# Kernel optimization log

Measured on AMD Instinct MI355X. Metric: run time of the kernel, lower is better.

Reference implementation:

```python
import jax, jax.numpy as jnp
import numpy as np

B, S, D = 4, 2048, 1024
H = 16
HD = D // H  # head dim = 64


def setup_inputs() -> dict:
    key = jax.random.key(0)
    ks = jax.random.split(key, 9)
    s = 1.0 / np.sqrt(D)
    return {
        "Q": jax.random.normal(ks[0], (B, S, D), dtype=jnp.float32),
        "K": jax.random.normal(ks[1], (B, S, D), dtype=jnp.float32),
        "V": jax.random.normal(ks[2], (B, S, D), dtype=jnp.float32),
        "Wq": jax.random.uniform(ks[3], (D, D), jnp.float32, -s, s),
        "bq": jax.random.uniform(ks[4], (D,), jnp.float32, -s, s),
        "Wk": jax.random.uniform(ks[5], (D, D), jnp.float32, -s, s),
        "bk": jax.random.uniform(ks[6], (D,), jnp.float32, -s, s),
        "Wv": jax.random.uniform(ks[7], (D, D), jnp.float32, -s, s),
        "bv": jax.random.uniform(ks[8], (D,), jnp.float32, -s, s),
    }


def reference(Q, K, V, Wq, bq, Wk, bk, Wv, bv):
    # Linear projections, split into heads: (B, H, S, HD)
    def proj(x, W, b):
        y = x @ W + b  # torch Linear uses x @ W.T; here W is stored pre-transposed (D_in, D_out)
        return y.reshape(B, S, H, HD).transpose(0, 2, 1, 3)

    q = proj(Q, Wq, bq)
    k = proj(K, Wk, bk)
    v = proj(V, Wv, bv)

    scale = 1.0 / jnp.sqrt(jnp.float32(HD))
    scores = jnp.einsum("bhqd,bhkd->bhqk", q, k) * scale  # (B,H,S,S)
    # causal mask (mask=True path): -inf above the diagonal
    causal = jnp.triu(jnp.full((S, S), -jnp.inf, dtype=scores.dtype), k=1)
    scores = scores + causal
    attn = jax.nn.softmax(scores, axis=-1)
    ctx = jnp.einsum("bhqk,bhkd->bhqd", attn, v)  # (B,H,S,HD)
    return ctx.transpose(0, 2, 1, 3).reshape(B, S, H * HD)
```

## Files before the change

### kernel.cpp

```cpp
#include <hip/hip_runtime.h>
#include <hip/hip_bf16.h>
#include <stdint.h>

#define B_  4
#define S_  2048
#define D_  1024
#define H_  16
#define HD_ 64
#define LOG2E 1.44269504088896f

typedef unsigned short u16;
typedef short bf16x8 __attribute__((ext_vector_type(8)));
typedef float f32x4 __attribute__((ext_vector_type(4)));

static __device__ __forceinline__ u16 f2bf(float f) {
    union { float f; uint32_t u; } v; v.f = f;
    return (u16)((v.u + 0x7FFF + ((v.u >> 16) & 1)) >> 16);
}

static __device__ __forceinline__ uint32_t cvt_pk_bf16(float lo, float hi) {
    uint32_t r;
    asm("v_cvt_pk_bf16_f32 %0, %1, %2" : "=v"(r) : "v"(lo), "v"(hi));
    return r;
}

static __device__ __forceinline__ uint32_t pk2(float lo, float hi) {
    return __builtin_amdgcn_perm(__float_as_uint(hi), __float_as_uint(lo), 0x07060302u);
}

static __device__ __forceinline__ bf16x8 rd_swz(const u16* base, int row, int slot) {
    return *(const bf16x8*)((const char*)base + row * 128 + ((slot ^ (row & 7)) << 4));
}

static __device__ __forceinline__ void gll_swz(const u16* grow0, size_t stride,
                                               u16* lds_chunk, int lane) {
    const int r = lane >> 3;
    const int slot = (lane & 7) ^ r;
    const u16* g = grow0 + (size_t)r * stride + slot * 8;
    __builtin_amdgcn_global_load_lds(
        (const __attribute__((address_space(1))) uint32_t*)g,
        (__attribute__((address_space(3))) uint32_t*)lds_chunk, 16, 0, 0);
}

__global__ __launch_bounds__(256) void wtrans(
    const float* __restrict__ W0, const float* __restrict__ W1, const float* __restrict__ W2,
    u16* __restrict__ T0, u16* __restrict__ T1, u16* __restrict__ T2)
{
    const float* W = blockIdx.z == 0 ? W0 : (blockIdx.z == 1 ? W1 : W2);
    u16* T       = blockIdx.z == 0 ? T0 : (blockIdx.z == 1 ? T1 : T2);
    __shared__ float t[32][33];
    const int n0 = blockIdx.x * 32, k0 = blockIdx.y * 32;
    const int tx = threadIdx.x, ty = threadIdx.y;
#pragma unroll
    for (int i = 0; i < 4; ++i)
        t[ty + i * 8][tx] = W[(size_t)(k0 + ty + i * 8) * D_ + n0 + tx];
    __syncthreads();
#pragma unroll
    for (int i = 0; i < 4; ++i)
        T[(size_t)(n0 + ty + i * 8) * D_ + k0 + tx] = f2bf(t[tx][ty + i * 8]);
}

template <int MODE>
__global__ __launch_bounds__(256) void proj_gemm(
    const float* __restrict__ X, const u16* __restrict__ Wt,
    const float* __restrict__ bias, u16* __restrict__ out)
{
    __shared__ __align__(16) u16 lA[128 * 64];
    __shared__ __align__(16) u16 lB[128 * 64];
    const int tid = threadIdx.x;
    const int m0 = blockIdx.x * 128, n0 = blockIdx.y * 128;
    const int w = tid >> 6, lane = tid & 63;
    const int lr = lane & 15, lg = lane >> 4;
    const int wr = (w >> 1) * 64, wc = (w & 1) * 64;

    f32x4 acc[4][4] = {};

    for (int k0 = 0; k0 < D_; k0 += 64) {
        __syncthreads();
#pragma unroll
        for (int i = 0; i < 4; ++i) {
            const int c = w * 4 + i;
            gll_swz(Wt + (size_t)(n0 + c * 8) * D_ + k0, D_, &lB[c * 512], lane);
        }
#pragma unroll
        for (int i = 0; i < 8; ++i) {
            const int lin = i * 1024 + tid * 4;
            const int r = lin >> 6, c = lin & 63;
            const float4 v = *(const float4*)(X + (size_t)(m0 + r) * D_ + k0 + c);
            uint2 pk;
            pk.x = pk2(v.x, v.y);
            pk.y = pk2(v.z, v.w);
            const int phys = r * 128 + (((c >> 3) ^ (r & 7)) << 4) + ((c & 7) << 1);
            *(uint2*)((char*)lA + phys) = pk;
        }
        __syncthreads();
#pragma unroll
        for (int kk = 0; kk < 64; kk += 32) {
            bf16x8 af[4], bfr[4];
#pragma unroll
            for (int m = 0; m < 4; ++m)
                af[m] = rd_swz(lA, wr + m * 16 + lr, (kk >> 3) + lg);
#pragma unroll
            for (int n = 0; n < 4; ++n)
                bfr[n] = rd_swz(lB, wc + n * 16 + lr, (kk >> 3) + lg);
#pragma unroll
            for (int m = 0; m < 4; ++m)
#pragma unroll
                for (int n = 0; n < 4; ++n)
                    acc[m][n] = __builtin_amdgcn_mfma_f32_16x16x32_bf16(af[m], bfr[n], acc[m][n], 0, 0, 0);
        }
    }
#pragma unroll
    for (int m = 0; m < 4; ++m)
#pragma unroll
        for (int n = 0; n < 4; ++n)
#pragma unroll
            for (int j = 0; j < 4; ++j) {
                const int gm = m0 + wr + m * 16 + lg * 4 + j;
                const int gn = n0 + wc + n * 16 + lr;
                float y = acc[m][n][j] + bias[gn];
                if (MODE == 0) y *= 0.125f * LOG2E;
                const int bb = gm >> 11, s = gm & (S_ - 1);
                const int h = gn >> 6, hd = gn & 63;
                size_t off;
                if (MODE < 2) off = (((size_t)bb * H_ + h) * S_ + s) * HD_ + hd;
                else {
                    const int s6 = s & 63;
                    const int sp = (s & ~63) | (s6 & 0x20) | ((s6 & 0xC) << 1) |
                                   ((s6 & 0x10) >> 2) | (s6 & 3);
                    off = (((size_t)bb * H_ + h) * HD_ + hd) * S_ + sp;
                }
                out[off] = f2bf(y);
            }
}

__global__ __launch_bounds__(512) void attn_kernel(
    const u16* __restrict__ qb, const u16* __restrict__ kb,
    const u16* __restrict__ vtb, float* __restrict__ out)
{
    const int bh = blockIdx.y;
    const int b = bh >> 4, h = bh & 15;
    const int tid = threadIdx.x;
    const int w = tid >> 6, lane = tid & 63;
    const int lr = lane & 15, lg = lane >> 4;

    __shared__ __align__(16) u16 lK[64 * 64];
    __shared__ __align__(16) u16 lV[64 * 64];

    const size_t kbase = (size_t)bh * S_ * HD_;
    const size_t vbase = (size_t)bh * HD_ * S_;

    for (int e = 0; e < 2; ++e) {
        const int qi = (e == 0) ? (int)blockIdx.x : 15 - (int)blockIdx.x;
        const int q0 = qi * 128;
        const int qrow = q0 + w * 16 + lr;

        const size_t qoff = ((size_t)bh * S_ + qrow) * HD_;
        const bf16x8 qf0 = *(const bf16x8*)(qb + qoff + lg * 8);
        const bf16x8 qf1 = *(const bf16x8*)(qb + qoff + 32 + lg * 8);

        f32x4 oacc[4] = {};
        float l_run = 0.f;

        const int tmax = 2 * qi + 1;
        for (int t = 0; t <= tmax; ++t) {
            const int kv0 = t * 64;
            __syncthreads();
            gll_swz(kb + kbase + (size_t)(kv0 + w * 8) * HD_, HD_, &lK[w * 512], lane);
            gll_swz(vtb + vbase + (size_t)(w * 8) * S_ + kv0, S_, &lV[w * 512], lane);
            __syncthreads();

            if (t == tmax && w < 4) continue;

            f32x4 sacc[4];
            __builtin_amdgcn_s_setprio(1);
#pragma unroll
            for (int n = 0; n < 4; ++n) {
                const bf16x8 k0f = rd_swz(lK, n * 16 + lr, lg);
                const bf16x8 k1f = rd_swz(lK, n * 16 + lr, 4 + lg);
                f32x4 z = {};
                z = __builtin_amdgcn_mfma_f32_16x16x32_bf16(k0f, qf0, z, 0, 0, 0);
                z = __builtin_amdgcn_mfma_f32_16x16x32_bf16(k1f, qf1, z, 0, 0, 0);
                sacc[n] = z;
            }
            __builtin_amdgcn_s_setprio(0);

            if (t >= tmax - 1) {
#pragma unroll
                for (int n = 0; n < 4; ++n)
#pragma unroll
                    for (int j = 0; j < 4; ++j)
                        if (kv0 + n * 16 + lg * 4 + j > qrow) sacc[n][j] = -1e30f;
            }

            float g[16];
#pragma unroll
            for (int n = 0; n < 4; ++n)
#pragma unroll
                for (int j = 0; j < 4; ++j) {
                    const float p = exp2f(sacc[n][j]);
                    sacc[n][j] = p;
                    g[n * 4 + j] = p;
                }
#pragma unroll
            for (int s = 8; s >= 1; s >>= 1)
#pragma unroll
                for (int k = 0; k < s; ++k) g[k] += g[k + s];
            float rs = g[0];
            rs += __shfl_xor(rs, 16);
            rs += __shfl_xor(rs, 32);
            l_run += rs;

            uint32_t pw[4][2];
#pragma unroll
            for (int n = 0; n < 4; ++n)
#pragma unroll
                for (int jh = 0; jh < 2; ++jh)
                    pw[n][jh] = cvt_pk_bf16(sacc[n][2 * jh], sacc[n][2 * jh + 1]);

            __builtin_amdgcn_s_setprio(1);
#pragma unroll
            for (int n = 0; n < 4; ++n) {
                const int row = n * 16 + lr;
#pragma unroll
                for (int m = 0; m < 2; ++m) {
                    const bf16x8 vf = rd_swz(lV, row, 4 * m + lg);
                    union { uint32_t u[4]; bf16x8 v; } af;
                    af.u[0] = pw[2 * m][0]; af.u[1] = pw[2 * m][1];
                    af.u[2] = pw[2 * m + 1][0]; af.u[3] = pw[2 * m + 1][1];
                    oacc[n] = __builtin_amdgcn_mfma_f32_16x16x32_bf16(af.v, vf, oacc[n], 0, 0, 0);
                }
            }
            __builtin_amdgcn_s_setprio(0);
        }

        const float inv = 1.f / l_run;
#pragma unroll
        for (int j = 0; j < 4; ++j) {
            const float iv = __shfl(inv, lg * 4 + j);
            const int row = q0 + w * 16 + lg * 4 + j;
#pragma unroll
            for (int n = 0; n < 4; ++n)
                out[((size_t)b * S_ + row) * D_ + h * HD_ + n * 16 + lr] = oacc[n][j] * iv;
        }
    }
}

extern "C" void kernel_launch(void* const* d_in, const int* in_sizes, int n_in,
                              void* d_out, int out_size, void* d_ws, size_t ws_size,
                              hipStream_t stream) {
    const float* Q  = (const float*)d_in[0];
    const float* K  = (const float*)d_in[1];
    const float* V  = (const float*)d_in[2];
    const float* Wq = (const float*)d_in[3];
    const float* bq = (const float*)d_in[4];
    const float* Wk = (const float*)d_in[5];
    const float* bk = (const float*)d_in[6];
    const float* Wv = (const float*)d_in[7];
    const float* bv = (const float*)d_in[8];
    float* out = (float*)d_out;

    char* ws = (char*)d_ws;
    const size_t WT_BYTES  = (size_t)D_ * D_ * 2;
    const size_t QKV_BYTES = (size_t)B_ * S_ * D_ * 2;
    u16* Wtq = (u16*)(ws);
    u16* Wtk = (u16*)(ws + WT_BYTES);
    u16* Wtv = (u16*)(ws + 2 * WT_BYTES);
    u16* qb  = (u16*)(ws + 3 * WT_BYTES);
    u16* kb  = (u16*)(ws + 3 * WT_BYTES + QKV_BYTES);
    u16* vtb = (u16*)(ws + 3 * WT_BYTES + 2 * QKV_BYTES);

    wtrans<<<dim3(32, 32, 3), dim3(32, 8), 0, stream>>>(Wq, Wk, Wv, Wtq, Wtk, Wtv);
    proj_gemm<0><<<dim3(64, 8), dim3(256), 0, stream>>>(Q, Wtq, bq, qb);
    proj_gemm<1><<<dim3(64, 8), dim3(256), 0, stream>>>(K, Wtk, bk, kb);
    proj_gemm<2><<<dim3(64, 8), dim3(256), 0, stream>>>(V, Wtv, bv, vtb);
    attn_kernel<<<dim3(8, B_ * H_), dim3(512), 0, stream>>>(qb, kb, vtb, out);
}
```

Baseline: 159.5 us.

## Load two KV tiles per barrier pair and compute row sums with MFMA

The attention loop now loads two 64-wide K/V tiles into separate LDS buffers between each pair of barriers, which halves the number of __syncthreads per query tile. The per-row softmax denominator is no longer built from a scalar add tree plus cross-lane shuffles. Instead it is accumulated by extra MFMAs that multiply the bf16 probabilities by a ones vector, so the row sum comes out in the same layout as the output accumulator. This trades two extra MFMAs per tile and doubled LDS use for less VALU and shuffle work. Because the denominator is now summed from the bf16-rounded probabilities, its numerics change slightly.

```diff
diff --git a/kernel.cpp b/kernel.cpp
--- a/kernel.cpp
+++ b/kernel.cpp
@@ -144,11 +144,16 @@
     const int w = tid >> 6, lane = tid & 63;
     const int lr = lane & 15, lg = lane >> 4;
 
-    __shared__ __align__(16) u16 lK[64 * 64];
-    __shared__ __align__(16) u16 lV[64 * 64];
+    __shared__ __align__(16) u16 lK0[64 * 64];
+    __shared__ __align__(16) u16 lV0[64 * 64];
+    __shared__ __align__(16) u16 lK1[64 * 64];
+    __shared__ __align__(16) u16 lV1[64 * 64];
 
     const size_t kbase = (size_t)bh * S_ * HD_;
     const size_t vbase = (size_t)bh * HD_ * S_;
+
+    union { uint32_t u[4]; bf16x8 v; } onesf;
+    onesf.u[0] = onesf.u[1] = onesf.u[2] = onesf.u[3] = 0x3F803F80u;
 
     for (int e = 0; e < 2; ++e) {
         const int qi = (e == 0) ? (int)blockIdx.x : 15 - (int)blockIdx.x;
@@ -160,18 +165,12 @@
         const bf16x8 qf1 = *(const bf16x8*)(qb + qoff + 32 + lg * 8);
 
         f32x4 oacc[4] = {};
-        float l_run = 0.f;
+        f32x4 lacc = {};
 
         const int tmax = 2 * qi + 1;
-        for (int t = 0; t <= tmax; ++t) {
+
+        auto compute = [&](int t, const u16* lK, const u16* lV) {
             const int kv0 = t * 64;
-            __syncthreads();
-            gll_swz(kb + kbase + (size_t)(kv0 + w * 8) * HD_, HD_, &lK[w * 512], lane);
-            gll_swz(vtb + vbase + (size_t)(w * 8) * S_ + kv0, S_, &lV[w * 512], lane);
-            __syncthreads();
-
-            if (t == tmax && w < 4) continue;
-
             f32x4 sacc[4];
             __builtin_amdgcn_s_setprio(1);
 #pragma unroll
@@ -193,55 +192,56 @@
                         if (kv0 + n * 16 + lg * 4 + j > qrow) sacc[n][j] = -1e30f;
             }
 
-            float g[16];
+            uint32_t pw[4][2];
 #pragma unroll
             for (int n = 0; n < 4; ++n)
 #pragma unroll
-                for (int j = 0; j < 4; ++j) {
-                    const float p = exp2f(sacc[n][j]);
-                    sacc[n][j] = p;
-                    g[n * 4 + j] = p;
-                }
-#pragma unroll
-            for (int s = 8; s >= 1; s >>= 1)
-#pragma unroll
-                for (int k = 0; k < s; ++k) g[k] += g[k + s];
-            float rs = g[0];
-            rs += __shfl_xor(rs, 16);
-            rs += __shfl_xor(rs, 32);
-            l_run += rs;
-
-            uint32_t pw[4][2];
-#pragma unroll
-            for (int n = 0; n < 4; ++n)
-#pragma unroll
                 for (int jh = 0; jh < 2; ++jh)
-                    pw[n][jh] = cvt_pk_bf16(sacc[n][2 * jh], sacc[n][2 * jh + 1]);
+                    pw[n][jh] = cvt_pk_bf16(exp2f(sacc[n][2 * jh]),
+                                            exp2f(sacc[n][2 * jh + 1]));
+
+            union { uint32_t u[4]; bf16x8 v; } a0, a1;
+            a0.u[0] = pw[0][0]; a0.u[1] = pw[0][1];
+            a0.u[2] = pw[1][0]; a0.u[3] = pw[1][1];
+            a1.u[0] = pw[2][0]; a1.u[1] = pw[2][1];
+            a1.u[2] = pw[3][0]; a1.u[3] = pw[3][1];
 
             __builtin_amdgcn_s_setprio(1);
 #pragma unroll
             for (int n = 0; n < 4; ++n) {
                 const int row = n * 16 + lr;
-#pragma unroll
-                for (int m = 0; m < 2; ++m) {
-                    const bf16x8 vf = rd_swz(lV, row, 4 * m + lg);
-                    union { uint32_t u[4]; bf16x8 v; } af;
-                    af.u[0] = pw[2 * m][0]; af.u[1] = pw[2 * m][1];
-                    af.u[2] = pw[2 * m + 1][0]; af.u[3] = pw[2 * m + 1][1];
-                    oacc[n] = __builtin_amdgcn_mfma_f32_16x16x32_bf16(af.v, vf, oacc[n], 0, 0, 0);
-                }
-            }
+                const bf16x8 vf0 = rd_swz(lV, row, lg);
+                const bf16x8 vf1 = rd_swz(lV, row, 4 + lg);
+                oacc[n] = __builtin_amdgcn_mfma_f32_16x16x32_bf16(a0.v, vf0, oacc[n], 0, 0, 0);
+                oacc[n] = __builtin_amdgcn_mfma_f32_16x16x32_bf16(a1.v, vf1, oacc[n], 0, 0, 0);
+            }
+            lacc = __builtin_amdgcn_mfma_f32_16x16x32_bf16(a0.v, onesf.v, lacc, 0, 0, 0);
+            lacc = __builtin_amdgcn_mfma_f32_16x16x32_bf16(a1.v, onesf.v, lacc, 0, 0, 0);
             __builtin_amdgcn_s_setprio(0);
-        }
-
-        const float inv = 1.f / l_run;
+        };
+
+        for (int tp = 0; tp <= tmax; tp += 2) {
+            const int kvA = tp * 64, kvB = kvA + 64;
+            __syncthreads();
+            gll_swz(kb + kbase + (size_t)(kvA + w * 8) * HD_, HD_, &lK0[w * 512], lane);
+            gll_swz(vtb + vbase + (size_t)(w * 8) * S_ + kvA, S_, &lV0[w * 512], lane);
+            gll_swz(kb + kbase + (size_t)(kvB + w * 8) * HD_, HD_, &lK1[w * 512], lane);
+            gll_swz(vtb + vbase + (size_t)(w * 8) * S_ + kvB, S_, &lV1[w * 512], lane);
+            __syncthreads();
+
+            compute(tp, lK0, lV0);
+            if (!(tp + 1 == tmax && w < 4)) compute(tp + 1, lK1, lV1);
+        }
+
+        f32x4 inv;
+#pragma unroll
+        for (int j = 0; j < 4; ++j) inv[j] = 1.f / lacc[j];
 #pragma unroll
         for (int j = 0; j < 4; ++j) {
-            const float iv = __shfl(inv, lg * 4 + j);
             const int row = q0 + w * 16 + lg * 4 + j;
 #pragma unroll
             for (int n = 0; n < 4; ++n)
-                out[((size_t)b * S_ + row) * D_ + h * HD_ + n * 16 + lr] = oacc[n][j] * iv;
+                out[((size_t)b * S_ + row) * D_ + h * HD_ + n * 16 + lr] = oacc[n][j] * inv[j];
         }
     }
 }
```

New measurement: 154.9 us. 2.9% less time.
